# Kernel optimization log

Hardware: AMD Instinct MI355X
Metric: run time of the kernel (lower is better)

The kernel has to match this reference:

```python
import jax, jax.numpy as jnp
import numpy as np

DIM = 10  # GMM components == feature dim


def _conv(x, w, b):
    y = jax.lax.conv_general_dilated(x, w, window_strides=(1, 1), padding='VALID',
                                     dimension_numbers=('NCHW', 'OIHW', 'NCHW'))
    return y + b[None, :, None, None]


def _gmm(x, centers, raw_mats):
    # x: [B, d]; centers: [K, d]; raw_mats: [K, d, d] with K == d == DIM
    K, d = centers.shape
    I = jnp.eye(d, dtype=x.dtype)
    L = jnp.tril(raw_mats, -1) + I                       # unit lower-triangular [K,d,d]
    root_D = jnp.diagonal(raw_mats, axis1=-2, axis2=-1)  # [K,d]
    D = root_D * root_D + 1e-4
    # Sigma_inv = L^{-T} D^{-1} L^{-1}
    L_inv = jax.scipy.linalg.solve_triangular(L, jnp.broadcast_to(I, L.shape), lower=True)
    Sigma_inv = jnp.einsum('kai,ka,kaj->kij', L_inv, 1.0 / D, L_inv)
    det_scale = jax.lax.rsqrt(jnp.prod(D, axis=-1))      # [K]
    diff = x[:, None, :] - centers[None, :, :]           # [B,K,d]
    dist_sq = jnp.einsum('bkd,kde,bke->bk', diff, Sigma_inv, diff)
    expo = -0.5 * dist_sq
    expo_safe = expo - jnp.max(expo, axis=1, keepdims=True)
    numer = det_scale[None, :] * jnp.exp(expo_safe)
    return numer / jnp.sum(numer, axis=1, keepdims=True)


def setup_inputs() -> dict:
    key = jax.random.key(0)
    ks = jax.random.split(key, 12)
    B = 4096
    x = jax.random.normal(ks[0], (B, 1, 28, 28), dtype=jnp.float32)
    conv1_w = jax.random.normal(ks[1], (32, 1, 3, 3), jnp.float32) * (1.0 / np.sqrt(1 * 9))
    conv1_b = jnp.zeros((32,), jnp.float32)
    conv2_w = jax.random.normal(ks[2], (64, 32, 3, 3), jnp.float32) * (1.0 / np.sqrt(32 * 9))
    conv2_b = jnp.zeros((64,), jnp.float32)
    fc1_w = jax.random.normal(ks[3], (128, 9216), jnp.float32) * (1.0 / np.sqrt(9216))
    fc1_b = jnp.zeros((128,), jnp.float32)
    fc2_w = jax.random.normal(ks[4], (DIM, 128), jnp.float32) * (1.0 / np.sqrt(128))
    fc2_b = jnp.zeros((DIM,), jnp.float32)
    centers = jax.random.normal(ks[5], (DIM, DIM), jnp.float32)
    raw_mats = jax.random.normal(ks[6], (DIM, DIM, DIM), jnp.float32) * 0.1 + jnp.eye(DIM)[None]
    return {'x': x, 'conv1_w': conv1_w, 'conv1_b': conv1_b, 'conv2_w': conv2_w,
            'conv2_b': conv2_b, 'fc1_w': fc1_w, 'fc1_b': fc1_b, 'fc2_w': fc2_w,
            'fc2_b': fc2_b, 'centers': centers, 'raw_mats': raw_mats}


def reference(x, conv1_w, conv1_b, conv2_w, conv2_b, fc1_w, fc1_b, fc2_w, fc2_b, centers, raw_mats):
    h = jax.nn.relu(_conv(x, conv1_w, conv1_b))          # [B,32,26,26]
    h = jax.nn.relu(_conv(h, conv2_w, conv2_b))          # [B,64,24,24]
    h = jax.lax.reduce_window(h, -jnp.inf, jax.lax.max, (1, 1, 2, 2), (1, 1, 2, 2), 'VALID')
    h = h.reshape(h.shape[0], -1)                        # [B,9216] (dropout = identity in eval)
    h = jax.nn.relu(h @ fc1_w.T + fc1_b)
    h = h @ fc2_w.T + fc2_b                              # [B,10]
    return _gmm(h, centers, raw_mats)
```

## Files before the change

### kernel.cpp

```cpp
#include <hip/hip_runtime.h>

typedef _Float16 half_t;
typedef _Float16 half8  __attribute__((ext_vector_type(8)));
typedef _Float16 half2v __attribute__((ext_vector_type(2)));
typedef float    floatx4 __attribute__((ext_vector_type(4)));

#define MFMA16(a, b, c) __builtin_amdgcn_mfma_f32_16x16x32_f16((a), (b), (c), 0, 0, 0)

__global__ void k_prep(const float* __restrict__ fw1, half_t* __restrict__ W1h,
                       const float* __restrict__ w2, half_t* __restrict__ W2T,
                       const float* __restrict__ raw, float* __restrict__ Sinv,
                       float* __restrict__ dets) {
    __shared__ float s_raw[1000];
    __shared__ float s_Li[1000];
    __shared__ float s_Dinv[100];
    const int blk = blockIdx.x;
    const int t = threadIdx.x;
    if (blk < 4608) {
        const int i = blk * 256 + t;
        W1h[i] = (half_t)fw1[i];
    } else if (blk < 4680) {
        const int i = (blk - 4608) * 256 + t;
        if (i < 18432) {
            const int tap = i / 2048;
            const int r = i - tap * 2048;
            const int co = r >> 5;
            const int ci = r & 31;
            W2T[i] = (half_t)w2[(co * 32 + ci) * 9 + tap];
        }
    } else {
        for (int i = t; i < 1000; i += 256) s_raw[i] = raw[i];
        __syncthreads();
        if (t < 100) {
            const int k = t / 10;
            const int j = t - k * 10;
            float v[10];
#pragma unroll
            for (int i = 0; i < 10; ++i) {
                float s = (i == j) ? 1.0f : 0.0f;
#pragma unroll
                for (int mm = 0; mm < 10; ++mm)
                    if (mm < i) s -= s_raw[k * 100 + i * 10 + mm] * v[mm];
                v[i] = s;
            }
#pragma unroll
            for (int a = 0; a < 10; ++a) s_Li[k * 100 + a * 10 + j] = v[a];
        } else if (t < 110) {
            const int k = t - 100;
            float prod = 1.0f;
#pragma unroll
            for (int a = 0; a < 10; ++a) {
                const float rd = s_raw[k * 100 + a * 10 + a];
                const float dv = rd * rd + 1e-4f;
                s_Dinv[k * 10 + a] = 1.0f / dv;
                prod *= dv;
            }
            dets[k] = rsqrtf(prod);
        }
        __syncthreads();
        for (int idx = t; idx < 1000; idx += 256) {
            const int k = idx / 100;
            const int r = idx - k * 100;
            const int ii = r / 10;
            const int jj = r - ii * 10;
            float s = 0.0f;
#pragma unroll
            for (int a = 0; a < 10; ++a)
                s += s_Li[k * 100 + a * 10 + ii] * s_Dinv[k * 10 + a] *
                     s_Li[k * 100 + a * 10 + jj];
            Sinv[idx] = s;
        }
    }
}

__global__ __launch_bounds__(256, 3) void k_convs(
    const float* __restrict__ x, const float* __restrict__ w1,
    const float* __restrict__ b1, const float* __restrict__ b2,
    const half_t* __restrict__ W2T, half_t* __restrict__ h2p) {
    __shared__ float s_x[784];
    __shared__ float s_w1[288];
    __shared__ float s_b1[32];
    __shared__ float s_b2[64];
    __shared__ __align__(16) half_t s_h1[21632];

    const int t = threadIdx.x;
    const int b = blockIdx.x;

    for (int i = t; i < 784; i += 256) s_x[i] = x[(size_t)b * 784 + i];
    for (int i = t; i < 288; i += 256) s_w1[i] = w1[i];
    if (t < 32) s_b1[t] = b1[t];
    if (t < 64) s_b2[t] = b2[t];
    __syncthreads();

    const int w = t >> 6;
    const int ln = t & 63;
    const int n16 = ln & 15;
    const int q = ln >> 4;

    {
        float wr[8][9], br[8];
#pragma unroll
        for (int j = 0; j < 8; ++j) {
            br[j] = s_b1[w * 8 + j];
#pragma unroll
            for (int k = 0; k < 9; ++k) wr[j][k] = s_w1[(w * 8 + j) * 9 + k];
        }
        for (int p = ln; p < 676; p += 64) {
            const int yy = p / 26;
            const int xx = p - yy * 26;
            float win[9];
#pragma unroll
            for (int r = 0; r < 3; ++r)
#pragma unroll
                for (int c = 0; c < 3; ++c) win[r * 3 + c] = s_x[(yy + r) * 28 + xx + c];
            half8 hv;
#pragma unroll
            for (int j = 0; j < 8; ++j) {
                float a = br[j];
#pragma unroll
                for (int k = 0; k < 9; ++k) a = fmaf(win[k], wr[j][k], a);
                hv[j] = (half_t)fmaxf(a, 0.0f);
            }
            const int off = ((p << 6) + (w << 4)) ^ ((p & 7) << 4);
            *(half8*)((char*)s_h1 + off) = hv;
        }
    }

    const int cp = w & 1;
    half8 bf[9][2];
#pragma unroll
    for (int tap = 0; tap < 9; ++tap)
#pragma unroll
        for (int cc = 0; cc < 2; ++cc)
            bf[tap][cc] = *(const half8*)(W2T +
                ((tap * 64 + (2 * cp + cc) * 16 + n16) * 32 + q * 8));

    __syncthreads();

#pragma unroll
    for (int tap = 0; tap < 9; ++tap)
#pragma unroll
        for (int cc = 0; cc < 2; ++cc)
            asm volatile("" : "+v"(bf[tap][cc]));

    const int am = ln & 15;
    const int aly = 2 * ((am >> 2) & 1) + ((am >> 1) & 1);
    const int alx = 2 * (am >> 3) + (am & 1);
    const int qoff = q << 4;
    const char* h1b = (const char*)s_h1;
    const int mhalf = w >> 1;

    for (int i = 0; i < 18; ++i) {
        const int mt = mhalf * 18 + i;
        const int tY = mt / 6;
        const int tX = mt - tY * 6;
        const int ybase = 4 * tY + aly;
        const int xbase = 4 * tX + alx;
        floatx4 acc0 = {0.f, 0.f, 0.f, 0.f};
        floatx4 acc1 = {0.f, 0.f, 0.f, 0.f};
#pragma unroll
        for (int tap = 0; tap < 9; ++tap) {
            const int ky = tap / 3;
            const int kx = tap - ky * 3;
            const int pix = (ybase + ky) * 26 + xbase + kx;
            const int off = ((pix << 6) + qoff) ^ ((pix & 7) << 4);
            const half8 af = *(const half8*)(h1b + off);
            acc0 = MFMA16(af, bf[tap][0], acc0);
            acc1 = MFMA16(af, bf[tap][1], acc1);
        }
        const int poolY = 2 * tY + (q & 1);
        const int poolX = 2 * tX + (q >> 1);
        const float v0 = fmaxf(fmaxf(acc0[0], acc0[1]), fmaxf(acc0[2], acc0[3]));
        const float v1 = fmaxf(fmaxf(acc1[0], acc1[1]), fmaxf(acc1[2], acc1[3]));
        const int co0 = (2 * cp) * 16 + n16;
        const int co1 = co0 + 16;
        const size_t base = (size_t)b * 9216 + poolY * 12 + poolX;
        h2p[base + (size_t)co0 * 144] = (half_t)fmaxf(v0 + s_b2[co0], 0.0f);
        h2p[base + (size_t)co1 * 144] = (half_t)fmaxf(v1 + s_b2[co1], 0.0f);
    }
}

__global__ __launch_bounds__(256) void k_fc1(const half_t* __restrict__ A,
                                             const half_t* __restrict__ W,
                                             half_t* __restrict__ part) {
    const int t = threadIdx.x;
    const int mb = blockIdx.x;
    const int kb = blockIdx.y;
    const int w = t >> 6, ln = t & 63, n16 = ln & 15, q = ln >> 4;

    const half_t* a0 = A + (size_t)(mb * 128 + w * 32 + n16) * 9216 + kb * 576 + q * 8;
    const half_t* a1 = a0 + (size_t)16 * 9216;
    const half_t* wp = W + (size_t)n16 * 9216 + kb * 576 + q * 8;

    floatx4 acc[2][8];
#pragma unroll
    for (int s = 0; s < 2; ++s)
#pragma unroll
        for (int nt = 0; nt < 8; ++nt) acc[s][nt] = (floatx4){0.f, 0.f, 0.f, 0.f};

    for (int kt = 0; kt < 18; ++kt) {
        const int ko = kt * 32;
        half8 af0 = *(const half8*)(a0 + ko);
        half8 af1 = *(const half8*)(a1 + ko);
#pragma unroll
        for (int nt = 0; nt < 8; ++nt) {
            half8 bfr = *(const half8*)(wp + (size_t)nt * 16 * 9216 + ko);
            acc[0][nt] = MFMA16(af0, bfr, acc[0][nt]);
            acc[1][nt] = MFMA16(af1, bfr, acc[1][nt]);
        }
    }
    const int rowbase = mb * 128 + w * 32;
#pragma unroll
    for (int s = 0; s < 2; ++s)
#pragma unroll
        for (int nt = 0; nt < 8; ++nt)
#pragma unroll
            for (int r = 0; r < 4; ++r) {
                const int row = rowbase + s * 16 + q * 4 + r;
                const int col = nt * 16 + n16;
                part[(size_t)kb * 524288 + (size_t)row * 128 + col] = (half_t)acc[s][nt][r];
            }
}

__global__ void k_fc1red(const half_t* __restrict__ part, const float* __restrict__ b,
                         half_t* __restrict__ h3) {
    const int idx = blockIdx.x * 256 + threadIdx.x;
    const int col = idx & 127;
    float s = 0.0f;
#pragma unroll
    for (int j = 0; j < 16; ++j) s += (float)part[(size_t)j * 524288 + idx];
    s = fmaxf(s + b[col], 0.0f);
    h3[idx] = (half_t)s;
}

__global__ __launch_bounds__(256) void k_fc2gmm(
    const half_t* __restrict__ h3, const float* __restrict__ fw,
    const float* __restrict__ fb, const float* __restrict__ cent,
    const float* __restrict__ Sinv, const float* __restrict__ dets,
    float* __restrict__ out) {
    __shared__ float sw[1280];
    __shared__ float sb[10];
    __shared__ float sc[100];
    __shared__ float ss[1000];
    __shared__ float sd[10];
    const int t = threadIdx.x;
    for (int i = t; i < 1280; i += 256) sw[i] = fw[i];
    if (t < 10) sb[t] = fb[t];
    if (t < 100) sc[t] = cent[t];
    for (int i = t; i < 1000; i += 256) ss[i] = Sinv[i];
    if (t < 10) sd[t] = dets[t];
    __syncthreads();

    const int bidx = blockIdx.x * 256 + t;
    half2v hh[64];
    const half2v* hp = (const half2v*)(h3 + (size_t)bidx * 128);
#pragma unroll
    for (int i = 0; i < 64; ++i) hh[i] = hp[i];

    float y[10];
#pragma unroll
    for (int o = 0; o < 10; ++o) {
        float a = sb[o];
#pragma unroll
        for (int k = 0; k < 64; ++k) {
            a = fmaf((float)hh[k][0], sw[o * 128 + 2 * k], a);
            a = fmaf((float)hh[k][1], sw[o * 128 + 2 * k + 1], a);
        }
        y[o] = a;
    }

    float expo[10];
    float mx = -3.402823466e38f;
#pragma unroll
    for (int k = 0; k < 10; ++k) {
        float d[10];
#pragma unroll
        for (int j = 0; j < 10; ++j) d[j] = y[j] - sc[k * 10 + j];
        float s = 0.0f;
#pragma unroll
        for (int i = 0; i < 10; ++i) {
            float r = 0.0f;
#pragma unroll
            for (int j = 0; j < 10; ++j) r = fmaf(ss[k * 100 + i * 10 + j], d[j], r);
            s = fmaf(d[i], r, s);
        }
        expo[k] = -0.5f * s;
        mx = fmaxf(mx, expo[k]);
    }
    float num[10];
    float sum = 0.0f;
#pragma unroll
    for (int k = 0; k < 10; ++k) {
        num[k] = sd[k] * __expf(expo[k] - mx);
        sum += num[k];
    }
    const float inv = 1.0f / sum;
#pragma unroll
    for (int k = 0; k < 10; ++k) out[(size_t)bidx * 10 + k] = num[k] * inv;
}

extern "C" void kernel_launch(void* const* d_in, const int* in_sizes, int n_in,
                              void* d_out, int out_size, void* d_ws, size_t ws_size,
                              hipStream_t stream) {
    const float* x = (const float*)d_in[0];
    const float* w1 = (const float*)d_in[1];
    const float* b1 = (const float*)d_in[2];
    const float* w2 = (const float*)d_in[3];
    const float* b2 = (const float*)d_in[4];
    const float* fw1 = (const float*)d_in[5];
    const float* fb1 = (const float*)d_in[6];
    const float* fw2 = (const float*)d_in[7];
    const float* fb2 = (const float*)d_in[8];
    const float* cen = (const float*)d_in[9];
    const float* raw = (const float*)d_in[10];
    float* out = (float*)d_out;

    char* ws = (char*)d_ws;
    half_t* W2T = (half_t*)(ws);
    half_t* W1h = (half_t*)(ws + 36864);
    half_t* h2p = (half_t*)(ws + 2396160);
    half_t* part = (half_t*)(ws + 77893632);
    half_t* h3h = (half_t*)(ws + 94670848);
    float* gS = (float*)(ws + 95719424);
    float* gD = (float*)(ws + 95723424);

    k_prep<<<4681, 256, 0, stream>>>(fw1, W1h, w2, W2T, raw, gS, gD);
    k_convs<<<4096, 256, 0, stream>>>(x, w1, b1, b2, W2T, h2p);
    k_fc1<<<dim3(32, 16), 256, 0, stream>>>(h2p, W1h, part);
    k_fc1red<<<2048, 256, 0, stream>>>(part, fb1, h3h);
    k_fc2gmm<<<16, 256, 0, stream>>>(h3h, fw2, fb2, cen, gS, gD, out);
}
```

Baseline: 261.2 us.

## Restructure conv2 MFMA as row-streaming with rolling accumulators and fused pooling

Conv2 changes from independent 4x4 pixel tiles, which reload nine shifted A fragments per tile, to a row-streaming scheme. Each wave walks input rows once, and each loaded row of three fragments feeds three rolling output-row accumulators, one per kernel row. The max-pool is done across row pairs held in registers, and results go out as half2 stores. The LDS XOR swizzle is dropped and the buffer padded with zeros so reads past the end stay in bounds, which cuts redundant LDS reads but may add bank conflicts and register pressure.

```diff
diff --git a/kernel.cpp b/kernel.cpp
--- a/kernel.cpp
+++ b/kernel.cpp
@@ -81,7 +81,7 @@
     __shared__ float s_w1[288];
     __shared__ float s_b1[32];
     __shared__ float s_b2[64];
-    __shared__ __align__(16) half_t s_h1[21632];
+    __shared__ __align__(16) half_t s_h1[688 * 32];
 
     const int t = threadIdx.x;
     const int b = blockIdx.x;
@@ -90,6 +90,7 @@
     for (int i = t; i < 288; i += 256) s_w1[i] = w1[i];
     if (t < 32) s_b1[t] = b1[t];
     if (t < 64) s_b2[t] = b2[t];
+    if (t < 384) s_h1[21632 + t] = (half_t)0.0f;
     __syncthreads();
 
     const int w = t >> 6;
@@ -121,12 +122,12 @@
                 for (int k = 0; k < 9; ++k) a = fmaf(win[k], wr[j][k], a);
                 hv[j] = (half_t)fmaxf(a, 0.0f);
             }
-            const int off = ((p << 6) + (w << 4)) ^ ((p & 7) << 4);
-            *(half8*)((char*)s_h1 + off) = hv;
+            *(half8*)((char*)s_h1 + ((p << 6) + (w << 4))) = hv;
         }
     }
 
     const int cp = w & 1;
+    const int st = w >> 1;
     half8 bf[9][2];
 #pragma unroll
     for (int tap = 0; tap < 9; ++tap)
@@ -143,41 +144,82 @@
         for (int cc = 0; cc < 2; ++cc)
             asm volatile("" : "+v"(bf[tap][cc]));
 
-    const int am = ln & 15;
-    const int aly = 2 * ((am >> 2) & 1) + ((am >> 1) & 1);
-    const int alx = 2 * (am >> 3) + (am & 1);
-    const int qoff = q << 4;
-    const char* h1b = (const char*)s_h1;
-    const int mhalf = w >> 1;
-
-    for (int i = 0; i < 18; ++i) {
-        const int mt = mhalf * 18 + i;
-        const int tY = mt / 6;
-        const int tX = mt - tY * 6;
-        const int ybase = 4 * tY + aly;
-        const int xbase = 4 * tX + alx;
-        floatx4 acc0 = {0.f, 0.f, 0.f, 0.f};
-        floatx4 acc1 = {0.f, 0.f, 0.f, 0.f};
-#pragma unroll
-        for (int tap = 0; tap < 9; ++tap) {
-            const int ky = tap / 3;
-            const int kx = tap - ky * 3;
-            const int pix = (ybase + ky) * 26 + xbase + kx;
-            const int off = ((pix << 6) + qoff) ^ ((pix & 7) << 4);
-            const half8 af = *(const half8*)(h1b + off);
-            acc0 = MFMA16(af, bf[tap][0], acc0);
-            acc1 = MFMA16(af, bf[tap][1], acc1);
-        }
-        const int poolY = 2 * tY + (q & 1);
-        const int poolX = 2 * tX + (q >> 1);
-        const float v0 = fmaxf(fmaxf(acc0[0], acc0[1]), fmaxf(acc0[2], acc0[3]));
-        const float v1 = fmaxf(fmaxf(acc1[0], acc1[1]), fmaxf(acc1[2], acc1[3]));
-        const int co0 = (2 * cp) * 16 + n16;
-        const int co1 = co0 + 16;
-        const size_t base = (size_t)b * 9216 + poolY * 12 + poolX;
-        h2p[base + (size_t)co0 * 144] = (half_t)fmaxf(v0 + s_b2[co0], 0.0f);
-        h2p[base + (size_t)co1 * 144] = (half_t)fmaxf(v1 + s_b2[co1], 0.0f);
-    }
+    const char* rp = (const char*)s_h1 + (((n16 + 16 * st) << 6) + (q << 4));
+
+    const float bb0 = s_b2[cp * 32 + n16];
+    const float bb1 = s_b2[cp * 32 + 16 + n16];
+    half_t* outp = h2p + (size_t)b * 9216 + (size_t)(cp * 32 + n16) * 144 +
+                   8 * st + 2 * q;
+    const bool dostore = (st == 0) | (q < 2);
+
+    const floatx4 z4 = {0.f, 0.f, 0.f, 0.f};
+    floatx4 sl0[2] = {z4, z4}, sl1[2] = {z4, z4}, sl2[2] = {z4, z4};
+    float yb00 = 0.f, yb01 = 0.f, yb10 = 0.f, yb11 = 0.f;
+
+#define RETIRE(YO, AC)                                                        \
+    do {                                                                      \
+        const float p0 = fmaxf(AC[0][0], AC[0][1]);                           \
+        const float p1 = fmaxf(AC[0][2], AC[0][3]);                           \
+        const float r0 = fmaxf(AC[1][0], AC[1][1]);                           \
+        const float r1 = fmaxf(AC[1][2], AC[1][3]);                           \
+        if (((YO) & 1) == 0) {                                                \
+            yb00 = p0; yb01 = p1; yb10 = r0; yb11 = r1;                       \
+        } else if (dostore) {                                                 \
+            half2v h0, h1v;                                                   \
+            h0[0] = (half_t)fmaxf(fmaxf(yb00, p0) + bb0, 0.0f);               \
+            h0[1] = (half_t)fmaxf(fmaxf(yb01, p1) + bb0, 0.0f);               \
+            h1v[0] = (half_t)fmaxf(fmaxf(yb10, r0) + bb1, 0.0f);              \
+            h1v[1] = (half_t)fmaxf(fmaxf(yb11, r1) + bb1, 0.0f);              \
+            half_t* op = outp + ((YO) >> 1) * 12;                             \
+            *(half2v*)(op) = h0;                                              \
+            *(half2v*)(op + 2304) = h1v;                                      \
+        }                                                                     \
+        AC[0] = z4; AC[1] = z4;                                               \
+    } while (0)
+
+#define CSTEP(Y_, A0, A1, A2)                                                 \
+    do {                                                                      \
+        const int y_ = (Y_);                                                  \
+        if (y_ < 26) {                                                        \
+            const half8 f0 = *(const half8*)(rp);                             \
+            const half8 f1 = *(const half8*)(rp + 64);                        \
+            const half8 f2 = *(const half8*)(rp + 128);                       \
+            if (y_ <= 23) {                 \
+                A0[0] = MFMA16(f0, bf[0][0], A0[0]);                          \
+                A0[1] = MFMA16(f0, bf[0][1], A0[1]);                          \
+                A0[0] = MFMA16(f1, bf[1][0], A0[0]);                          \
+                A0[1] = MFMA16(f1, bf[1][1], A0[1]);                          \
+                A0[0] = MFMA16(f2, bf[2][0], A0[0]);                          \
+                A0[1] = MFMA16(f2, bf[2][1], A0[1]);                          \
+            }                                                                 \
+            if (y_ >= 1 && y_ <= 24) {    \
+                A1[0] = MFMA16(f0, bf[3][0], A1[0]);                          \
+                A1[1] = MFMA16(f0, bf[3][1], A1[1]);                          \
+                A1[0] = MFMA16(f1, bf[4][0], A1[0]);                          \
+                A1[1] = MFMA16(f1, bf[4][1], A1[1]);                          \
+                A1[0] = MFMA16(f2, bf[5][0], A1[0]);                          \
+                A1[1] = MFMA16(f2, bf[5][1], A1[1]);                          \
+            }                                                                 \
+            if (y_ >= 2) {   \
+                A2[0] = MFMA16(f0, bf[6][0], A2[0]);                          \
+                A2[1] = MFMA16(f0, bf[6][1], A2[1]);                          \
+                A2[0] = MFMA16(f1, bf[7][0], A2[0]);                          \
+                A2[1] = MFMA16(f1, bf[7][1], A2[1]);                          \
+                A2[0] = MFMA16(f2, bf[8][0], A2[0]);                          \
+                A2[1] = MFMA16(f2, bf[8][1], A2[1]);                          \
+                RETIRE(y_ - 2, A2);                                           \
+            }                                                                 \
+            rp += 1664;                                                       \
+        }                                                                     \
+    } while (0)
+
+    for (int yb = 0; yb < 27; yb += 3) {
+        CSTEP(yb + 0, sl0, sl2, sl1);
+        CSTEP(yb + 1, sl1, sl0, sl2);
+        CSTEP(yb + 2, sl2, sl1, sl0);
+    }
+#undef CSTEP
+#undef RETIRE
 }
 
 __global__ __launch_bounds__(256) void k_fc1(const half_t* __restrict__ A,
```

Measured after the change: 242.0 us. 7.4% less time.
